# Optimization experiments

Hardware: AMD Instinct MI355X
Metric: run time of the kernel (lower is better)

The kernel has to match this reference:

```python
import jax, jax.numpy as jnp
from jax import lax
import numpy as np

B, N, NPOINT, NSAMPLE, RADIUS = 8, 16384, 1024, 32, 0.4
C_IN = 64


def fps(xyz, npoint):
    """Furthest point sampling. xyz: (B, N, 3) -> (B, npoint) int32 indices.
    Matches the CUDA kernel: start from index 0, iteratively pick argmax of
    the running min-distance to the selected set."""
    Bb, Nn, _ = xyz.shape

    def step(carry, _):
        min_d, last = carry
        p = jnp.take_along_axis(xyz, last[:, None, None], axis=1)  # (B,1,3)
        d = jnp.sum((xyz - p) ** 2, axis=-1)                       # (B,N)
        min_d = jnp.minimum(min_d, d)
        nxt = jnp.argmax(min_d, axis=1).astype(jnp.int32)
        return (min_d, nxt), nxt

    idx0 = jnp.zeros((Bb,), jnp.int32)
    min_d0 = jnp.full((Bb, Nn), jnp.inf, xyz.dtype)
    _, rest = lax.scan(step, (min_d0, idx0), None, length=npoint - 1)  # (npoint-1, B)
    return jnp.transpose(jnp.concatenate([idx0[None, :], rest], axis=0))  # (B, npoint)


def ball_query(xyz, new_xyz, radius, nsample):
    """xyz: (B,N,3), new_xyz: (B,P,3) -> (B,P,nsample) int32 indices.
    First nsample in-radius indices (ascending), short balls padded with the
    first found index (the centroid itself is always in-radius)."""
    Nn = xyz.shape[1]
    d2 = jnp.sum((new_xyz[:, :, None, :] - xyz[:, None, :, :]) ** 2, axis=-1)  # (B,P,N)
    ar = jnp.arange(Nn, dtype=jnp.int32)
    key = jnp.where(d2 <= radius * radius, ar, Nn)  # out-of-ball -> sentinel N
    neg_top, _ = lax.top_k(-key, nsample)           # nsample smallest keys
    gidx = -neg_top                                  # (B,P,nsample)
    return jnp.where(gidx == Nn, gidx[..., :1], gidx)


def setup_inputs() -> dict:
    key = jax.random.key(0)
    ks = jax.random.split(key, 8)
    return {
        "xyz": jax.random.normal(ks[0], (B, N, 3), jnp.float32),
        "features": jax.random.normal(ks[1], (B, C_IN, N), jnp.float32),
        "W1": jax.random.normal(ks[2], (64, 3 + C_IN), jnp.float32) * 0.05,
        "b1": jax.random.normal(ks[3], (64,), jnp.float32) * 0.05,
        "W2": jax.random.normal(ks[4], (64, 64), jnp.float32) * 0.05,
        "b2": jax.random.normal(ks[5], (64,), jnp.float32) * 0.05,
        "W3": jax.random.normal(ks[6], (128, 64), jnp.float32) * 0.05,
        "b3": jax.random.normal(ks[7], (128,), jnp.float32) * 0.05,
    }


def reference(xyz, features, W1, b1, W2, b2, W3, b3):
    Bb = xyz.shape[0]
    idx = fps(xyz, NPOINT)                                         # (B,P)
    new_xyz = jnp.take_along_axis(xyz, idx[:, :, None], axis=1)    # (B,P,3)

    gidx = ball_query(xyz, new_xyz, RADIUS, NSAMPLE)               # (B,P,S)
    bi = jnp.arange(Bb)[:, None, None]
    grouped_xyz = xyz[bi, gidx] - new_xyz[:, :, None, :]           # (B,P,S,3) relative coords
    feats_t = jnp.transpose(features, (0, 2, 1))                   # (B,N,C)
    grouped_feats = feats_t[bi, gidx]                              # (B,P,S,C)
    h = jnp.concatenate([grouped_xyz, grouped_feats], axis=-1)     # (B,P,S,3+C)

    # shared per-point MLP (1x1 convs) + ReLU
    h = jax.nn.relu(jnp.einsum('bpsc,oc->bpso', h, W1) + b1)
    h = jax.nn.relu(jnp.einsum('bpsc,oc->bpso', h, W2) + b2)
    h = jax.nn.relu(jnp.einsum('bpsc,oc->bpso', h, W3) + b3)

    pooled = jnp.max(h, axis=2)                                    # (B,P,128) max over nsample
    new_features = jnp.transpose(pooled, (0, 2, 1))                # (B,128,P)
    return new_xyz, new_features
```

## Files before the change

### kernel.cpp

```cpp
#include <hip/hip_runtime.h>

#define R2 0.16f

typedef float f32x2 __attribute__((ext_vector_type(2)));

__device__ __forceinline__ float sqd(float x, float y, float z,
                                     float px, float py, float pz) {
  float dx = __fsub_rn(x, px);
  float dy = __fsub_rn(y, py);
  float dz = __fsub_rn(z, pz);
  return __fadd_rn(__fadd_rn(__fmul_rn(dx, dx), __fmul_rn(dy, dy)),
                   __fmul_rn(dz, dz));
}

__device__ __forceinline__ float wave64_max_dpp(float x) {
#define DPP_STEP(CTRL)                                                      \
  {                                                                         \
    int t_ = __builtin_amdgcn_update_dpp(__float_as_int(x),                 \
                                         __float_as_int(x), CTRL, 0xf, 0xf, \
                                         false);                            \
    x = fmaxf(x, __int_as_float(t_));                                       \
  }
  DPP_STEP(0x111) DPP_STEP(0x112) DPP_STEP(0x114)
  DPP_STEP(0x118) DPP_STEP(0x142) DPP_STEP(0x143)
#undef DPP_STEP
  return x;
}
__device__ __forceinline__ unsigned wave64_min_dpp_u32(unsigned x) {
#define DPP_STEP(CTRL)                                                      \
  {                                                                         \
    unsigned t_ = (unsigned)__builtin_amdgcn_update_dpp(                    \
        (int)x, (int)x, CTRL, 0xf, 0xf, false);                             \
    x = (t_ < x) ? t_ : x;                                                  \
  }
  DPP_STEP(0x111) DPP_STEP(0x112) DPP_STEP(0x114)
  DPP_STEP(0x118) DPP_STEP(0x142) DPP_STEP(0x143)
#undef DPP_STEP
  return x;
}

__global__ __launch_bounds__(256) void zero_hist(unsigned* __restrict__ h) {
  h[blockIdx.x * 256 + threadIdx.x] = 0u;
}

__global__ __launch_bounds__(256) void hist_kernel(const float* __restrict__ xyz,
                                                   unsigned* __restrict__ hist,
                                                   unsigned* __restrict__ rank,
                                                   unsigned* __restrict__ cid) {
  int t = blockIdx.x * 256 + threadIdx.x;
  int b = t >> 14;
  const float* p = xyz + (size_t)t * 3;
  int cx = (int)floorf(p[0] + 4.0f);
  int cy = (int)floorf(p[1] + 4.0f);
  int cz = (int)floorf(p[2] + 4.0f);
  cx = min(max(cx, 0), 7);
  cy = min(max(cy, 0), 7);
  cz = min(max(cz, 0), 7);
  unsigned c = (unsigned)(cx | (cy << 3) | (cz << 6));
  unsigned r = atomicAdd(&hist[(b << 9) + c], 1u);
  rank[t] = r;
  cid[t] = c;
}

__global__ __launch_bounds__(512) void scan_kernel(const unsigned* __restrict__ hist,
                                                   unsigned* __restrict__ starts) {
  __shared__ unsigned a[512];
  int b = blockIdx.x, t = threadIdx.x;
  unsigned h = hist[(b << 9) + t];
  a[t] = h;
  __syncthreads();
  for (int s = 1; s < 512; s <<= 1) {
    unsigned v = (t >= s) ? a[t - s] : 0u;
    __syncthreads();
    a[t] += v;
    __syncthreads();
  }
  starts[(b << 9) + t] = a[t] - h;
}

__global__ __launch_bounds__(256) void scatter_kernel(
    const float* __restrict__ xyz, const unsigned* __restrict__ starts,
    const unsigned* __restrict__ rank, const unsigned* __restrict__ cid,
    float* __restrict__ xs2, float* __restrict__ ys2, float* __restrict__ zs2,
    unsigned* __restrict__ oi2) {
  int t = blockIdx.x * 256 + threadIdx.x;
  int b = t >> 14, n = t & 16383;
  unsigned pos = starts[(b << 9) + cid[t]] + rank[t];
  const float* p = xyz + (size_t)t * 3;
  size_t o = ((size_t)b << 14) + pos;
  xs2[o] = p[0];
  ys2[o] = p[1];
  zs2[o] = p[2];
  oi2[o] = (unsigned)n;
}

__global__ __launch_bounds__(1024) void fps_kernel(
    const float* __restrict__ xyz, const float* __restrict__ xs,
    const float* __restrict__ ys, const float* __restrict__ zs,
    const unsigned* __restrict__ oi, int* __restrict__ idx_out) {
#pragma clang fp contract(off)
  extern __shared__ float4 xylds[];
  __shared__ unsigned long long s_gkey[3];
  __shared__ float s_cd[3][3][16];
  int b = blockIdx.x;
  int tid = threadIdx.x;
  int lane = tid & 63, wid = tid >> 6;
  const float* xb = xyz + (size_t)b * 16384 * 3;
  int base = tid << 4;
  const float4* xv = (const float4*)(xs + ((size_t)b << 14) + base);
  const float4* yv = (const float4*)(ys + ((size_t)b << 14) + base);
  const float4* zv = (const float4*)(zs + ((size_t)b << 14) + base);
  const uint4* ov = (const uint4*)(oi + ((size_t)b << 14) + base);
  float xr[16], yr[16], zr[16];
  unsigned OI[16];
#pragma unroll
  for (int q = 0; q < 4; ++q) {
    *(float4*)(xr + 4 * q) = xv[q];
    *(float4*)(yr + 4 * q) = yv[q];
    *(float4*)(zr + 4 * q) = zv[q];
    *(uint4*)(OI + 4 * q) = ov[q];
  }
  float bxl = xr[0], bxh = xr[0], byl = yr[0], byh = yr[0], bzl = zr[0],
        bzh = zr[0];
#pragma unroll
  for (int k = 1; k < 16; ++k) {
    bxl = fminf(bxl, xr[k]); bxh = fmaxf(bxh, xr[k]);
    byl = fminf(byl, yr[k]); byh = fmaxf(byh, yr[k]);
    bzl = fminf(bzl, zr[k]); bzh = fmaxf(bzh, zr[k]);
  }
  f32x2 Z[8], M[8];
#pragma unroll
  for (int q = 0; q < 8; ++q) {
    xylds[(q << 10) + tid] =
        make_float4(xr[2 * q], xr[2 * q + 1], yr[2 * q], yr[2 * q + 1]);
    Z[q] = {zr[2 * q], zr[2 * q + 1]};
    M[q] = {__builtin_inff(), __builtin_inff()};
  }
  if (tid == 0) idx_out[b * 1024] = 0;
  if (tid < 3) s_gkey[tid] = 0ull;
  __syncthreads();
  float px = xb[0], py = xb[1], pz = xb[2];
  float tv = __builtin_inff();
  for (int it = 1; it < 1024; ++it) {
    int sl = it % 3;
    int slp2 = (sl + 2) % 3;
    float ddx = fmaxf(fmaxf(bxl - px, px - bxh), 0.0f);
    float ddy = fmaxf(fmaxf(byl - py, py - byh), 0.0f);
    float ddz = fmaxf(fmaxf(bzl - pz, pz - bzh), 0.0f);
    float lb = (ddx * ddx + ddy * ddy + ddz * ddz) * 0.999f;
    if (lb < tv) {
      f32x2 px2 = {px, px}, py2 = {py, py}, pz2 = {pz, pz};
      float ntv = -1.0f;
#pragma unroll
      for (int q = 0; q < 8; ++q) {
        float4 t = xylds[(q << 10) + tid];
        f32x2 X = {t.x, t.y};
        f32x2 Y = {t.z, t.w};
        f32x2 dx = X - px2;
        f32x2 dy = Y - py2;
        f32x2 dz = Z[q] - pz2;
        f32x2 d = dx * dx + dy * dy + dz * dz;
        M[q].x = fminf(M[q].x, d.x);
        M[q].y = fminf(M[q].y, d.y);
        ntv = fmaxf(fmaxf(ntv, M[q].x), M[q].y);
      }
      tv = ntv;
    }
    float bv = wave64_max_dpp(tv);
    unsigned bvb = (unsigned)__builtin_amdgcn_readlane(__float_as_int(bv), 63);
    float bvf = __int_as_float((int)bvb);
    unsigned long long gk0 = __hip_atomic_load(
        &s_gkey[sl], __ATOMIC_RELAXED, __HIP_MEMORY_SCOPE_WORKGROUP);
    if (bvb >= (unsigned)(gk0 >> 18)) {
      unsigned coi = 0xffffffffu;
      float wx = 0.0f, wy = 0.0f, wz = 0.0f;
      if (tv == bvf) {
#pragma unroll
        for (int q = 0; q < 8; ++q) {
          float4 t = xylds[(q << 10) + tid];
          if (M[q].x == bvf && OI[2 * q] < coi) {
            coi = OI[2 * q]; wx = t.x; wy = t.z; wz = Z[q].x;
          }
          if (M[q].y == bvf && OI[2 * q + 1] < coi) {
            coi = OI[2 * q + 1]; wx = t.y; wy = t.w; wz = Z[q].y;
          }
        }
      }
      unsigned woi = wave64_min_dpp_u32(coi);
      if (coi == woi && coi != 0xffffffffu) {
        s_cd[sl][0][wid] = wx;
        s_cd[sl][1][wid] = wy;
        s_cd[sl][2][wid] = wz;
        unsigned long long key = ((unsigned long long)bvb << 18) |
                                 ((unsigned long long)(16383u - woi) << 4) |
                                 (unsigned long long)wid;
        atomicMax(&s_gkey[sl], key);
      }
    }
    __syncthreads();
    unsigned long long gk = s_gkey[sl];
    if (tid == 0) s_gkey[slp2] = 0ull;
    int w2 = (int)(gk & 15ull);
    int j = 16383 - (int)((gk >> 4) & 0x3fffull);
    px = s_cd[sl][0][w2];
    py = s_cd[sl][1][w2];
    pz = s_cd[sl][2][w2];
    if (tid == 0) idx_out[b * 1024 + it] = j;
  }
}

__global__ __launch_bounds__(256) void gather_newxyz(const float* __restrict__ xyz,
                                                     const int* __restrict__ idx,
                                                     float* __restrict__ out) {
  int t = blockIdx.x * 256 + threadIdx.x;
  int b = t >> 10;
  int i = idx[t];
  const float* src = xyz + ((size_t)b * 16384 + i) * 3;
  float* dst = out + (size_t)t * 3;
  dst[0] = src[0];
  dst[1] = src[1];
  dst[2] = src[2];
}

__global__ __launch_bounds__(256) void transpose_feats(const float* __restrict__ f,
                                                       float* __restrict__ fT) {
  __shared__ float tile[64][65];
  int b = blockIdx.x >> 8;
  int n0 = (blockIdx.x & 255) << 6;
  int t = threadIdx.x;
  int nn = t & 63, c0 = t >> 6;
#pragma unroll
  for (int r = 0; r < 64; r += 4) {
    int c = c0 + r;
    tile[c][nn] = f[((size_t)b * 64 + c) * 16384 + n0 + nn];
  }
  __syncthreads();
  int cc = t & 63, n1 = t >> 6;
#pragma unroll
  for (int r = 0; r < 64; r += 4) {
    int n = n1 + r;
    fT[((size_t)b * 16384 + n0 + n) * 64 + cc] = tile[cc][n];
  }
}

__global__ __launch_bounds__(256) void ballquery_kernel(const float* __restrict__ xyz,
                                                        const float* __restrict__ newxyz,
                                                        int* __restrict__ gidx) {
  int wid = threadIdx.x >> 6, lane = threadIdx.x & 63;
  int cid = blockIdx.x * 4 + wid;
  int b = cid >> 10;
  const float* xb = xyz + (size_t)b * 16384 * 3;
  float cx = newxyz[cid * 3 + 0];
  float cy = newxyz[cid * 3 + 1];
  float cz = newxyz[cid * 3 + 2];
  int* out = gidx + (size_t)cid * 32;
  int found = 0;
  int first = -1;
  for (int c0 = 0; c0 < 16384; c0 += 64) {
    int g = c0 + lane;
    float xx = xb[g * 3 + 0], yy = xb[g * 3 + 1], zz = xb[g * 3 + 2];
    float d2 = sqd(xx, yy, zz, cx, cy, cz);
    bool inr = (d2 <= R2);
    unsigned long long mask = __ballot(inr);
    if (first < 0 && mask) first = c0 + (int)__builtin_ctzll(mask);
    int pre = __popcll(mask & ((1ull << lane) - 1ull));
    int slot = found + pre;
    if (inr && slot < 32) out[slot] = g;
    found += __popcll(mask);
    if (found >= 32) break;
  }
  for (int s = found + lane; s < 32; s += 64) out[s] = first;
}

#define FMA16(BASEPTR)                                                     \
  do {                                                                     \
    const float4* hp_ = (const float4*)(BASEPTR);                          \
    float4 v0 = hp_[0], v1 = hp_[1], v2 = hp_[2], v3 = hp_[3];             \
    float a = acc[s];                                                      \
    a = fmaf(w[0], v0.x, a);  a = fmaf(w[1], v0.y, a);                     \
    a = fmaf(w[2], v0.z, a);  a = fmaf(w[3], v0.w, a);                     \
    a = fmaf(w[4], v1.x, a);  a = fmaf(w[5], v1.y, a);                     \
    a = fmaf(w[6], v1.z, a);  a = fmaf(w[7], v1.w, a);                     \
    a = fmaf(w[8], v2.x, a);  a = fmaf(w[9], v2.y, a);                     \
    a = fmaf(w[10], v2.z, a); a = fmaf(w[11], v2.w, a);                    \
    a = fmaf(w[12], v3.x, a); a = fmaf(w[13], v3.y, a);                    \
    a = fmaf(w[14], v3.z, a); a = fmaf(w[15], v3.w, a);                    \
    acc[s] = a;                                                            \
  } while (0)

__global__ __launch_bounds__(256) void mlp_kernel(
    const float* __restrict__ xyz, const float* __restrict__ feats,
    const float* __restrict__ featsT, const float* __restrict__ newxyz,
    const int* __restrict__ gidx,
    const float* __restrict__ W1, const float* __restrict__ b1,
    const float* __restrict__ W2, const float* __restrict__ b2,
    const float* __restrict__ W3, const float* __restrict__ b3,
    float* __restrict__ out, int useT) {
  __shared__ float buf[4][32 * 68];
  int wid = threadIdx.x >> 6, lane = threadIdx.x & 63;
  int cid = blockIdx.x * 4 + wid;
  int b = cid >> 10, p = cid & 1023;
  float* A = buf[wid];
  const int* gi = gidx + (size_t)cid * 32;
  float cx = newxyz[cid * 3 + 0];
  float cy = newxyz[cid * 3 + 1];
  float cz = newxyz[cid * 3 + 2];

  if (useT) {
    const float4* fT4 = (const float4*)(featsT + (size_t)b * 16384 * 64);
    for (int t = lane; t < 512; t += 64) {
      int s = t >> 4, q = t & 15;
      int g = gi[s];
      float4 v = fT4[(size_t)g * 16 + q];
      *(float4*)(A + s * 68 + q * 4) = v;
    }
  } else {
    const float* fb = feats + (size_t)b * 64 * 16384;
    for (int t = lane; t < 2048; t += 64) {
      int c = t >> 5, s = t & 31;
      int g = gi[s];
      A[s * 68 + c] = fb[(size_t)c * 16384 + g];
    }
  }
  for (int t = lane; t < 96; t += 64) {
    int s = t / 3, c = t - s * 3;
    int g = gi[s];
    float pv = xyz[((size_t)b * 16384 + g) * 3 + c];
    float cv = (c == 0) ? cx : ((c == 1) ? cy : cz);
    A[s * 68 + 64 + c] = __fsub_rn(pv, cv);
  }
  if (lane < 32) A[lane * 68 + 67] = 0.0f;
  __syncthreads();

  int o = lane;
  float acc[32];

#pragma unroll
  for (int s = 0; s < 32; ++s) acc[s] = b1[o];
  {
    const float* wr = W1 + o * 67;
    for (int cb = 0; cb < 4; ++cb) {
      float w[16];
#pragma unroll
      for (int q = 0; q < 16; ++q) w[q] = wr[3 + cb * 16 + q];
#pragma unroll
      for (int s = 0; s < 32; ++s) { FMA16(A + s * 68 + cb * 16); }
    }
    float w0 = wr[0], w1 = wr[1], w2 = wr[2];
#pragma unroll
    for (int s = 0; s < 32; ++s) {
      float a = acc[s];
      a = fmaf(w0, A[s * 68 + 64], a);
      a = fmaf(w1, A[s * 68 + 65], a);
      a = fmaf(w2, A[s * 68 + 66], a);
      acc[s] = a;
    }
  }
  __syncthreads();
#pragma unroll
  for (int s = 0; s < 32; ++s) A[s * 64 + o] = fmaxf(acc[s], 0.0f);
  __syncthreads();

#pragma unroll
  for (int s = 0; s < 32; ++s) acc[s] = b2[o];
  {
    const float* wr = W2 + o * 64;
    for (int cb = 0; cb < 4; ++cb) {
      float w[16];
#pragma unroll
      for (int q = 0; q < 16; ++q) w[q] = wr[cb * 16 + q];
#pragma unroll
      for (int s = 0; s < 32; ++s) { FMA16(A + s * 64 + cb * 16); }
    }
  }
  __syncthreads();
#pragma unroll
  for (int s = 0; s < 32; ++s) A[s * 64 + o] = fmaxf(acc[s], 0.0f);
  __syncthreads();

  float* outp = out + 24576;
  for (int po = 0; po < 2; ++po) {
    int o2 = lane + (po << 6);
#pragma unroll
    for (int s = 0; s < 32; ++s) acc[s] = b3[o2];
    const float* wr = W3 + o2 * 64;
    for (int cb = 0; cb < 4; ++cb) {
      float w[16];
#pragma unroll
      for (int q = 0; q < 16; ++q) w[q] = wr[cb * 16 + q];
#pragma unroll
      for (int s = 0; s < 32; ++s) { FMA16(A + s * 64 + cb * 16); }
    }
    float mx = 0.0f;
#pragma unroll
    for (int s = 0; s < 32; ++s) mx = fmaxf(mx, acc[s]);
    outp[((size_t)b * 128 + o2) * 1024 + p] = mx;
  }
}

extern "C" void kernel_launch(void* const* d_in, const int* in_sizes, int n_in,
                              void* d_out, int out_size, void* d_ws, size_t ws_size,
                              hipStream_t stream) {
  const float* xyz = (const float*)d_in[0];
  const float* feats = (const float*)d_in[1];
  const float* W1 = (const float*)d_in[2];
  const float* b1 = (const float*)d_in[3];
  const float* W2 = (const float*)d_in[4];
  const float* b2 = (const float*)d_in[5];
  const float* W3 = (const float*)d_in[6];
  const float* b3 = (const float*)d_in[7];
  float* out = (float*)d_out;

  char* w = (char*)d_ws;
  int* idx = (int*)w;
  int* gidx = (int*)(w + 32768);
  unsigned* hist = (unsigned*)(w + 1081344);
  unsigned* starts = (unsigned*)(w + 1097728);
  unsigned* rank = (unsigned*)(w + 1114112);
  unsigned* cid = (unsigned*)(w + 1638400);
  unsigned* oi2 = (unsigned*)(w + 2162688);
  float* xs2 = (float*)(w + 2686976);
  float* ys2 = (float*)(w + 3211264);
  float* zs2 = (float*)(w + 3735552);
  float* featsT = (float*)(w + 4259840);
  size_t needT = 4259840 + (size_t)8 * 16384 * 64 * sizeof(float);
  int useT = (ws_size >= needT) ? 1 : 0;

  zero_hist<<<16, 256, 0, stream>>>(hist);
  hist_kernel<<<512, 256, 0, stream>>>(xyz, hist, rank, cid);
  scan_kernel<<<8, 512, 0, stream>>>(hist, starts);
  scatter_kernel<<<512, 256, 0, stream>>>(xyz, starts, rank, cid, xs2, ys2,
                                          zs2, oi2);
  fps_kernel<<<8, 1024, 131072, stream>>>(xyz, xs2, ys2, zs2, oi2, idx);
  gather_newxyz<<<32, 256, 0, stream>>>(xyz, idx, out);
  if (useT) transpose_feats<<<2048, 256, 0, stream>>>(feats, featsT);
  ballquery_kernel<<<2048, 256, 0, stream>>>(xyz, out, gidx);
  mlp_kernel<<<2048, 256, 0, stream>>>(xyz, feats, featsT, out, gidx,
                                       W1, b1, W2, b2, W3, b3, out, useT);
}
```

Baseline: 2.070 ms.

## Use spatial grid cells for ball query with per-centroid bitmask ordering

Replaces the linear scan over all points with a search over the voxel grid cells (8x8x8 over [-4,4]) that overlap the query sphere. It reuses the cell-sorted coordinates built earlier for FPS, and records in-radius hits in a shared-memory bitmask indexed by original point index. A wave-level prefix scan over that bitmask then emits the first 32 indices in ascending order. The aim is to cut distance evaluations, at the cost of atomics in shared memory and a full 16384-bit scan per centroid. It also relies on points outside the grid range being clamped into border cells.

```diff
diff --git a/kernel.cpp b/kernel.cpp
--- a/kernel.cpp
+++ b/kernel.cpp
@@ -243,33 +243,80 @@
   }
 }
 
-__global__ __launch_bounds__(256) void ballquery_kernel(const float* __restrict__ xyz,
-                                                        const float* __restrict__ newxyz,
-                                                        int* __restrict__ gidx) {
+__global__ __launch_bounds__(256) void ballquery_grid(
+    const float* __restrict__ xs, const float* __restrict__ ys,
+    const float* __restrict__ zs, const unsigned* __restrict__ oi,
+    const unsigned* __restrict__ hist, const unsigned* __restrict__ starts,
+    const float* __restrict__ newxyz, int* __restrict__ gidx) {
+  __shared__ unsigned bm[4][512];
+  __shared__ unsigned sfirst[4];
   int wid = threadIdx.x >> 6, lane = threadIdx.x & 63;
   int cid = blockIdx.x * 4 + wid;
   int b = cid >> 10;
-  const float* xb = xyz + (size_t)b * 16384 * 3;
   float cx = newxyz[cid * 3 + 0];
   float cy = newxyz[cid * 3 + 1];
   float cz = newxyz[cid * 3 + 2];
+  unsigned* mybm = bm[wid];
+#pragma unroll
+  for (int k = 0; k < 8; ++k) mybm[(k << 6) + lane] = 0u;
+  int clox = min(max((int)floorf(cx - 0.4f + 4.0f), 0), 7);
+  int chix = min(max((int)floorf(cx + 0.4f + 4.0f), 0), 7);
+  int cloy = min(max((int)floorf(cy - 0.4f + 4.0f), 0), 7);
+  int chiy = min(max((int)floorf(cy + 0.4f + 4.0f), 0), 7);
+  int cloz = min(max((int)floorf(cz - 0.4f + 4.0f), 0), 7);
+  int chiz = min(max((int)floorf(cz + 0.4f + 4.0f), 0), 7);
+  const float* xsb = xs + ((size_t)b << 14);
+  const float* ysb = ys + ((size_t)b << 14);
+  const float* zsb = zs + ((size_t)b << 14);
+  const unsigned* oib = oi + ((size_t)b << 14);
+  const unsigned* hb = hist + (b << 9);
+  const unsigned* sb = starts + (b << 9);
+  for (int zz = cloz; zz <= chiz; ++zz)
+    for (int yy = cloy; yy <= chiy; ++yy)
+      for (int xx = clox; xx <= chix; ++xx) {
+        unsigned cc = (unsigned)(xx | (yy << 3) | (zz << 6));
+        unsigned st = sb[cc], cnt = hb[cc];
+        for (unsigned c0 = 0; c0 < cnt; c0 += 64) {
+          unsigned g = c0 + (unsigned)lane;
+          if (g < cnt) {
+            unsigned p = st + g;
+            float d2 = sqd(xsb[p], ysb[p], zsb[p], cx, cy, cz);
+            if (d2 <= R2) {
+              unsigned o = oib[p];
+              atomicOr(&mybm[o >> 5], 1u << (o & 31));
+            }
+          }
+        }
+      }
   int* out = gidx + (size_t)cid * 32;
-  int found = 0;
-  int first = -1;
-  for (int c0 = 0; c0 < 16384; c0 += 64) {
-    int g = c0 + lane;
-    float xx = xb[g * 3 + 0], yy = xb[g * 3 + 1], zz = xb[g * 3 + 2];
-    float d2 = sqd(xx, yy, zz, cx, cy, cz);
-    bool inr = (d2 <= R2);
-    unsigned long long mask = __ballot(inr);
-    if (first < 0 && mask) first = c0 + (int)__builtin_ctzll(mask);
-    int pre = __popcll(mask & ((1ull << lane) - 1ull));
-    int slot = found + pre;
-    if (inr && slot < 32) out[slot] = g;
-    found += __popcll(mask);
-    if (found >= 32) break;
-  }
-  for (int s = found + lane; s < 32; s += 64) out[s] = first;
+  unsigned running = 0;
+  for (int s = 0; s < 4 && running < 32; ++s) {
+    unsigned lo = mybm[(s << 7) + 2 * lane];
+    unsigned hi = mybm[(s << 7) + 2 * lane + 1];
+    unsigned long long W = ((unsigned long long)hi << 32) | lo;
+    int c = __popcll(W);
+    int incl = c;
+#pragma unroll
+    for (int d = 1; d < 64; d <<= 1) {
+      int t = __shfl_up(incl, d);
+      if (lane >= d) incl += t;
+    }
+    int total = __shfl(incl, 63);
+    int basep = (int)running + incl - c;
+    while (W != 0ull && basep < 32) {
+      int t = (int)__builtin_ctzll(W);
+      W &= W - 1ull;
+      int idxv = (((s << 6) + lane) << 6) + t;
+      if (basep == 0) sfirst[wid] = (unsigned)idxv;
+      out[basep] = idxv;
+      ++basep;
+    }
+    running += (unsigned)total;
+  }
+  unsigned nf = running < 32u ? running : 32u;
+  unsigned first = sfirst[wid];
+  for (unsigned s2 = nf + (unsigned)lane; s2 < 32u; s2 += 64u)
+    out[s2] = (int)first;
 }
 
 #define FMA16(BASEPTR)                                                     \
@@ -434,7 +481,8 @@
   fps_kernel<<<8, 1024, 131072, stream>>>(xyz, xs2, ys2, zs2, oi2, idx);
   gather_newxyz<<<32, 256, 0, stream>>>(xyz, idx, out);
   if (useT) transpose_feats<<<2048, 256, 0, stream>>>(feats, featsT);
-  ballquery_kernel<<<2048, 256, 0, stream>>>(xyz, out, gidx);
+  ballquery_grid<<<2048, 256, 0, stream>>>(xs2, ys2, zs2, oi2, hist, starts,
+                                           out, gidx);
   mlp_kernel<<<2048, 256, 0, stream>>>(xyz, feats, featsT, out, gidx,
                                        W1, b1, W2, b2, W3, b3, out, useT);
 }
```

After: 1.999 ms. 3.4% less time.
